# Performance work log

Hardware: AMD Instinct MI355X
Metric: run time of the kernel (lower is better)

The kernel has to match this reference:

```python
import jax, jax.numpy as jnp
import numpy as np

# ---- static synthetic forest: 64 complete binary trees, depth 9 (heap layout) ----
DEPTH = 9
N_TREES = 64
C = 8
M = 256
N_GEN = 8
NPT = 2 ** (DEPTH + 1) - 1          # 1023 nodes per tree
DIM = N_TREES * NPT                  # 65472 total nodes
_base = np.arange(N_TREES) * NPT

def _lvl_nodes(l):
    return (_base[:, None] + np.arange(2 ** l - 1, 2 ** (l + 1) - 1)[None, :]).reshape(-1)

LEVELS = []   # list of (parent_idx, child_idx) edge arrays, top level first
UPAR = []     # unique parents per level (== nodes of level l-1)
for _l in range(1, DEPTH + 1):
    _ch = np.arange(2 ** _l - 1, 2 ** (_l + 1) - 1)
    _pa = (_ch - 1) // 2
    LEVELS.append((jnp.asarray((_base[:, None] + _pa[None, :]).reshape(-1)),
                   jnp.asarray((_base[:, None] + _ch[None, :]).reshape(-1))))
    UPAR.append(jnp.asarray(_lvl_nodes(_l - 1)))
LEAVES = jnp.asarray(_lvl_nodes(DEPTH))
ROOTS = jnp.asarray(_base)
INTERNAL = jnp.asarray(np.concatenate([_lvl_nodes(l) for l in range(DEPTH)]))
TREES_IND = jnp.asarray(np.repeat(np.arange(N_TREES), NPT))
N_CH = 2.0  # every internal node has exactly 2 children -> segment mean = sum/2


def _forward(A, B, Pi, x):
    # softmax reparameterization (per generative head)
    sm_A = jax.nn.softmax(A, axis=0)          # (C,C,G), softmax over parent-state dim 0
    sm_B = jax.nn.softmax(B, axis=1)          # (C,M,G), softmax over symbols
    sm_Pi = jax.nn.softmax(Pi, axis=0)        # (C,G)

    # B[:, x] gathered per node, as (node, C, G)
    B_x = jnp.transpose(sm_B[:, x], (1, 0, 2))  # (DIM,C,G)

    # ---- reversed upward (leaves -> roots) ----
    beta = jnp.zeros((DIM, C, N_GEN), dtype=A.dtype)
    t_beta = jnp.zeros((DIM, C, N_GEN), dtype=A.dtype)
    b_leaf = sm_Pi[None, :, :] * B_x[LEAVES]                 # (L,C,G)
    beta = beta.at[LEAVES].set(b_leaf / b_leaf.sum(1, keepdims=True))
    for (pa, ch), upar in zip(reversed(LEVELS), reversed(UPAR)):
        beta_ch = beta[ch]                                   # (E,C,G)
        t_beta_ch = jnp.einsum('ijg,ejg->eig', sm_A, beta_ch)
        t_beta = t_beta + jax.ops.segment_sum(t_beta_ch, pa, num_segments=DIM) / N_CH
        beta_l = t_beta[upar] * B_x[upar]                    # (U,C,G)
        beta = beta.at[upar].set(beta_l / beta_l.sum(1, keepdims=True))

    # ---- reversed downward (roots -> leaves) ----
    eps = jnp.zeros((DIM, C, N_GEN), dtype=A.dtype)
    t_eps = jnp.zeros((DIM, C, C, N_GEN), dtype=A.dtype)
    eps = eps.at[ROOTS].set(beta[ROOTS])
    for pa, ch in LEVELS:
        # (E,Cpa,Cch,G)
        eps_joint = (eps[pa][:, :, None, :] * sm_A[None]
                     * beta[ch][:, None, :, :] / t_beta[pa][:, :, None, :])
        t_eps = t_eps + jax.ops.segment_sum(eps_joint, pa, num_segments=DIM) / N_CH
        eps = eps.at[ch].set(eps_joint.sum(1))

    # ---- log-likelihood ----
    lik = jnp.zeros((DIM, N_GEN), dtype=A.dtype)
    lik = lik.at[INTERNAL].add((t_eps[INTERNAL] * jnp.log(sm_A)[None]).sum((1, 2)))
    lik = lik + (eps * jnp.log(B_x)).sum(1)  # all_nodes == all nodes here
    lik = lik.at[LEAVES].add((eps[LEAVES] * jnp.log(sm_Pi)[None]).sum(1))
    ll = jax.ops.segment_sum(lik, TREES_IND, num_segments=N_TREES)  # (n_trees,G)
    return -ll


def setup_inputs() -> dict:
    key = jax.random.key(0)
    k1, k2, k3, k4 = jax.random.split(key, 4)
    A = jax.random.uniform(k1, (C, C, N_GEN), minval=-5.0, maxval=5.0)
    B = jax.random.uniform(k2, (C, M, N_GEN), minval=-5.0, maxval=5.0)
    Pi = jax.random.uniform(k3, (C, N_GEN), minval=-5.0, maxval=5.0)
    x = jax.random.randint(k4, (DIM,), 0, M)
    return {"A": A, "B": B, "Pi": Pi, "x": x}


def reference(A, B, Pi, x):
    return _forward(A, B, Pi, x)
```

## Files before the change

kernel.cpp:

```cpp
#include <hip/hip_runtime.h>

#define NT 256

namespace {
constexpr int C = 8, G = 8, M = 256, NPT = 1023;
constexpr int PD = 12;

__device__ __forceinline__ float rcpf(float x) { return __builtin_amdgcn_rcpf(x); }

#define LD8(dst, srcp) do {                                              \
    const float4 _a = *(const float4*)(srcp);                            \
    const float4 _b = *(const float4*)((srcp) + 4);                      \
    (dst)[0]=_a.x;(dst)[1]=_a.y;(dst)[2]=_a.z;(dst)[3]=_a.w;             \
    (dst)[4]=_b.x;(dst)[5]=_b.y;(dst)[6]=_b.z;(dst)[7]=_b.w; } while(0)

#define ST8(dstp, src) do {                                              \
    *(float4*)(dstp)       = make_float4((src)[0],(src)[1],(src)[2],(src)[3]); \
    *(float4*)((dstp) + 4) = make_float4((src)[4],(src)[5],(src)[6],(src)[7]); } while(0)

__global__ __launch_bounds__(NT, 2)
void htmm_fused(const float* __restrict__ Ag, const float* __restrict__ Bg,
                const float* __restrict__ Pig, const int* __restrict__ xg,
                float* __restrict__ out)
{
    __shared__ int xs[NPT + 1];
    __shared__ __align__(16) float smBt[M][PD];
    __shared__ __align__(16) float logBt[M][PD];
    __shared__ __align__(16) float bet[511][PD];
    __shared__ __align__(16) float tbe[255][PD];
    __shared__ __align__(16) float smA_s[C][C];
    __shared__ __align__(16) float alA_s[C][C];
    __shared__ float pi_s[2][C];
    __shared__ float red[4];

    const int tid  = threadIdx.x;
    const int wv   = tid >> 6, lane = tid & 63;
    const int tree = blockIdx.x >> 3, g = blockIdx.x & 7;

    for (int n = tid; n < NPT; n += NT) xs[n] = xg[tree * NPT + n];
    {
        const int i  = 2 * wv + (lane >> 5);
        const int c0 = lane & 31;
        float raw[8], ex[8], ssum = 0.f;
        #pragma unroll
        for (int t = 0; t < 8; ++t) {
            raw[t] = Bg[(i * M + c0 + 32 * t) * G + g];
            ex[t]  = __expf(raw[t]);
            ssum  += ex[t];
        }
        #pragma unroll
        for (int m = 1; m <= 16; m <<= 1) ssum += __shfl_xor(ssum, m);
        const float inv = rcpf(ssum), ls = __logf(ssum);
        #pragma unroll
        for (int t = 0; t < 8; ++t) {
            smBt [c0 + 32 * t][i] = ex[t] * inv;
            logBt[c0 + 32 * t][i] = raw[t] - ls;
        }
    }
    if (wv == 0) {
        const int si = lane >> 3, qj = lane & 7;
        const float raw = Ag[(si * C + qj) * G + g];
        float e = __expf(raw), S = e;
        #pragma unroll
        for (int m = 8; m <= 32; m <<= 1) S += __shfl_xor(S, m);
        const float v = e / S;
        smA_s[si][qj] = v;
        alA_s[si][qj] = v * (raw - __logf(S));
    } else if (wv == 1 && lane < C) {
        const float raw = Pig[lane * G + g];
        float e = __expf(raw), S = e;
        #pragma unroll
        for (int m = 1; m <= 4; m <<= 1) S += __shfl_xor(S, m);
        pi_s[0][lane] = e / S;
        pi_s[1][lane] = raw - __logf(S);
    }
    __syncthreads();

    float Ae[64], ALAe[64], piR[8], lPi[8];
    #pragma unroll
    for (int i = 0; i < 8; ++i) {
        float ar[8], lr[8];
        LD8(ar, &smA_s[i][0]);
        LD8(lr, &alA_s[i][0]);
        #pragma unroll
        for (int j = 0; j < 8; ++j) { Ae[8*i+j] = ar[j]; ALAe[8*i+j] = lr[j]; }
    }
    #pragma unroll
    for (int i = 0; i < 8; ++i) { piR[i] = pi_s[0][i]; lPi[i] = pi_s[1][i]; }

    const int nd8 = 255 + tid;
    const int xv8 = xs[nd8], xvL = xs[2*nd8 + 1], xvR = xs[2*nd8 + 2];
    float bl0[8], bl1[8], tb8[8], b8[8];
    {
        float sm[8], u[8], S, inv;
        LD8(sm, &smBt[xvL][0]);
        S = 0.f;
        #pragma unroll
        for (int i = 0; i < 8; ++i) { u[i] = piR[i] * sm[i]; S += u[i]; }
        inv = rcpf(S);
        #pragma unroll
        for (int i = 0; i < 8; ++i) bl0[i] = u[i] * inv;

        LD8(sm, &smBt[xvR][0]);
        S = 0.f;
        #pragma unroll
        for (int i = 0; i < 8; ++i) { u[i] = piR[i] * sm[i]; S += u[i]; }
        inv = rcpf(S);
        #pragma unroll
        for (int i = 0; i < 8; ++i) bl1[i] = u[i] * inv;

        float c[8];
        #pragma unroll
        for (int j = 0; j < 8; ++j) c[j] = bl0[j] + bl1[j];
        #pragma unroll
        for (int i = 0; i < 8; ++i) {
            float t = 0.f;
            #pragma unroll
            for (int j = 0; j < 8; ++j) t += Ae[8*i+j] * c[j];
            tb8[i] = 0.5f * t;
        }
        LD8(sm, &smBt[xv8][0]);
        S = 0.f;
        #pragma unroll
        for (int i = 0; i < 8; ++i) { u[i] = tb8[i] * sm[i]; S += u[i]; }
        inv = rcpf(S);
        #pragma unroll
        for (int i = 0; i < 8; ++i) b8[i] = u[i] * inv;
        ST8(&bet[nd8][0], b8);
    }
    __syncthreads();

    for (int lvl = 7; lvl >= 0; --lvl) {
        const int cnt = 1 << lvl, base = cnt - 1;
        if (tid < cnt) {
            const int p = base + tid, cl = 2*p + 1;
            float lb_[8], rb_[8], cb[8];
            LD8(lb_, &bet[cl][0]);
            LD8(rb_, &bet[cl + 1][0]);
            #pragma unroll
            for (int j = 0; j < 8; ++j) cb[j] = lb_[j] + rb_[j];
            float tb[8];
            #pragma unroll
            for (int i = 0; i < 8; ++i) {
                float t = 0.f;
                #pragma unroll
                for (int j = 0; j < 8; ++j) t += Ae[8*i+j] * cb[j];
                tb[i] = 0.5f * t;
            }
            ST8(&tbe[p][0], tb);
            float sm[8], u[8], S = 0.f;
            LD8(sm, &smBt[xs[p]][0]);
            #pragma unroll
            for (int i = 0; i < 8; ++i) { u[i] = tb[i] * sm[i]; S += u[i]; }
            const float inv = rcpf(S);
            float b[8];
            #pragma unroll
            for (int i = 0; i < 8; ++i) b[i] = u[i] * inv;
            ST8(&bet[p][0], b);
        }
        __syncthreads();
    }

    float acc = 0.f;
    if (tid == 0) {
        float b0[8], lb[8];
        LD8(b0, &bet[0][0]);
        LD8(lb, &logBt[xs[0]][0]);
        #pragma unroll
        for (int j = 0; j < 8; ++j) acc += b0[j] * lb[j];
    }

    for (int dc = 1; dc <= 7; ++dc) {
        const int cnt = 1 << dc, base = cnt - 1;
        if (tid < cnt) {
            const int ch = base + tid, p = (ch - 1) >> 1;
            float ep[8], tp[8], w[8];
            LD8(ep, &bet[p][0]);
            LD8(tp, &tbe[p][0]);
            #pragma unroll
            for (int i = 0; i < 8; ++i) w[i] = ep[i] * rcpf(tp[i]);
            float es[8] = {0,0,0,0,0,0,0,0}, ts[8] = {0,0,0,0,0,0,0,0};
            #pragma unroll
            for (int i = 0; i < 8; ++i) {
                #pragma unroll
                for (int j = 0; j < 8; ++j) {
                    es[j] += w[i] * Ae[8*i+j];
                    ts[j] += w[i] * ALAe[8*i+j];
                }
            }
            float bc[8], lb[8], ev[8];
            LD8(bc, &bet[ch][0]);
            LD8(lb, &logBt[xs[ch]][0]);
            float a1 = 0.f, a2 = 0.f;
            #pragma unroll
            for (int j = 0; j < 8; ++j) {
                ev[j] = bc[j] * es[j];
                a1 += bc[j] * ts[j];
                a2 += ev[j] * lb[j];
            }
            acc += 0.5f * a1 + a2;
            ST8(&bet[ch][0], ev);
        }
        __syncthreads();
    }

    {
        const int p7 = (nd8 - 1) >> 1;
        float ep[8], tp[8], w[8];
        LD8(ep, &bet[p7][0]);
        LD8(tp, &tbe[p7][0]);
        #pragma unroll
        for (int i = 0; i < 8; ++i) w[i] = ep[i] * rcpf(tp[i]);
        float es[8] = {0,0,0,0,0,0,0,0}, ts[8] = {0,0,0,0,0,0,0,0};
        #pragma unroll
        for (int i = 0; i < 8; ++i) {
            #pragma unroll
            for (int j = 0; j < 8; ++j) {
                es[j] += w[i] * Ae[8*i+j];
                ts[j] += w[i] * ALAe[8*i+j];
            }
        }
        float lb[8], ev8[8], w8[8];
        LD8(lb, &logBt[xv8][0]);
        float a1 = 0.f, a2 = 0.f;
        #pragma unroll
        for (int j = 0; j < 8; ++j) {
            ev8[j] = b8[j] * es[j];
            a1 += b8[j] * ts[j];
            a2 += ev8[j] * lb[j];
        }
        acc += 0.5f * a1 + a2;
        #pragma unroll
        for (int i = 0; i < 8; ++i) w8[i] = ev8[i] * rcpf(tb8[i]);

        float es2[8] = {0,0,0,0,0,0,0,0}, ts2[8] = {0,0,0,0,0,0,0,0};
        #pragma unroll
        for (int i = 0; i < 8; ++i) {
            #pragma unroll
            for (int j = 0; j < 8; ++j) {
                es2[j] += w8[i] * Ae[8*i+j];
                ts2[j] += w8[i] * ALAe[8*i+j];
            }
        }
        LD8(lb, &logBt[xvL][0]);
        a1 = 0.f; a2 = 0.f;
        #pragma unroll
        for (int j = 0; j < 8; ++j) {
            const float ev = bl0[j] * es2[j];
            a1 += bl0[j] * ts2[j];
            a2 += ev * (lb[j] + lPi[j]);
        }
        acc += 0.5f * a1 + a2;
        LD8(lb, &logBt[xvR][0]);
        a1 = 0.f; a2 = 0.f;
        #pragma unroll
        for (int j = 0; j < 8; ++j) {
            const float ev = bl1[j] * es2[j];
            a1 += bl1[j] * ts2[j];
            a2 += ev * (lb[j] + lPi[j]);
        }
        acc += 0.5f * a1 + a2;
    }

    #pragma unroll
    for (int m = 1; m <= 32; m <<= 1) acc += __shfl_xor(acc, m);
    if (lane == 0) red[wv] = acc;
    __syncthreads();
    if (tid == 0) out[blockIdx.x] = -(red[0] + red[1] + red[2] + red[3]);
}
}

extern "C" void kernel_launch(void* const* d_in, const int* in_sizes, int n_in,
                              void* d_out, int out_size, void* d_ws, size_t ws_size,
                              hipStream_t stream) {
    const float* A  = (const float*)d_in[0];
    const float* Bm = (const float*)d_in[1];
    const float* Pi = (const float*)d_in[2];
    const int*   x  = (const int*)d_in[3];
    float* o = (float*)d_out;
    hipLaunchKernelGGL(htmm_fused, dim3(64 * 8), dim3(NT), 0, stream,
                       A, Bm, Pi, x, o);
}
```

Measured before the change: 90.02 us.

## Read transition matrices from LDS instead of registers and process child pairs per parent

Stops holding the 64-entry A and log-A matrices in per-thread registers and reads rows from shared memory (broadcast) inside helper lambdas, which should cut register pressure. The downward pass now has one thread per parent handle both children, so the weighted expectation (es/ts) is computed once per parent instead of twice. The trade-off is more LDS traffic per matrix-vector product, and the downward pass uses half as many active threads per level.

```diff
diff --git a/kernel.cpp b/kernel.cpp
--- a/kernel.cpp
+++ b/kernel.cpp
@@ -76,22 +76,36 @@
     }
     __syncthreads();
 
-    float Ae[64], ALAe[64], piR[8], lPi[8];
-    #pragma unroll
-    for (int i = 0; i < 8; ++i) {
-        float ar[8], lr[8];
-        LD8(ar, &smA_s[i][0]);
-        LD8(lr, &alA_s[i][0]);
-        #pragma unroll
-        for (int j = 0; j < 8; ++j) { Ae[8*i+j] = ar[j]; ALAe[8*i+j] = lr[j]; }
-    }
-    #pragma unroll
-    for (int i = 0; i < 8; ++i) { piR[i] = pi_s[0][i]; lPi[i] = pi_s[1][i]; }
+    auto trans_up = [&](const float* c8, float* tb) {
+        #pragma unroll
+        for (int i = 0; i < 8; ++i) {
+            float r[8]; LD8(r, &smA_s[i][0]);
+            float t = 0.f;
+            #pragma unroll
+            for (int j = 0; j < 8; ++j) t += r[j] * c8[j];
+            tb[i] = 0.5f * t;
+        }
+    };
+    auto wexp = [&](const float* w, float* es, float* ts) {
+        #pragma unroll
+        for (int j = 0; j < 8; ++j) { es[j] = 0.f; ts[j] = 0.f; }
+        #pragma unroll
+        for (int i = 0; i < 8; ++i) {
+            float a[8], l[8];
+            LD8(a, &smA_s[i][0]);
+            LD8(l, &alA_s[i][0]);
+            #pragma unroll
+            for (int j = 0; j < 8; ++j) { es[j] += w[i] * a[j]; ts[j] += w[i] * l[j]; }
+        }
+    };
+
+    float acc = 0.f;
 
     const int nd8 = 255 + tid;
     const int xv8 = xs[nd8], xvL = xs[2*nd8 + 1], xvR = xs[2*nd8 + 2];
     float bl0[8], bl1[8], tb8[8], b8[8];
     {
+        float piR[8]; LD8(piR, &pi_s[0][0]);
         float sm[8], u[8], S, inv;
         LD8(sm, &smBt[xvL][0]);
         S = 0.f;
@@ -112,13 +126,7 @@
         float c[8];
         #pragma unroll
         for (int j = 0; j < 8; ++j) c[j] = bl0[j] + bl1[j];
-        #pragma unroll
-        for (int i = 0; i < 8; ++i) {
-            float t = 0.f;
-            #pragma unroll
-            for (int j = 0; j < 8; ++j) t += Ae[8*i+j] * c[j];
-            tb8[i] = 0.5f * t;
-        }
+        trans_up(c, tb8);
         LD8(sm, &smBt[xv8][0]);
         S = 0.f;
         #pragma unroll
@@ -134,19 +142,12 @@
         const int cnt = 1 << lvl, base = cnt - 1;
         if (tid < cnt) {
             const int p = base + tid, cl = 2*p + 1;
-            float lb_[8], rb_[8], cb[8];
+            float lb_[8], rb_[8], cb[8], tb[8];
             LD8(lb_, &bet[cl][0]);
             LD8(rb_, &bet[cl + 1][0]);
             #pragma unroll
             for (int j = 0; j < 8; ++j) cb[j] = lb_[j] + rb_[j];
-            float tb[8];
-            #pragma unroll
-            for (int i = 0; i < 8; ++i) {
-                float t = 0.f;
-                #pragma unroll
-                for (int j = 0; j < 8; ++j) t += Ae[8*i+j] * cb[j];
-                tb[i] = 0.5f * t;
-            }
+            trans_up(cb, tb);
             ST8(&tbe[p][0], tb);
             float sm[8], u[8], S = 0.f;
             LD8(sm, &smBt[xs[p]][0]);
@@ -161,7 +162,6 @@
         __syncthreads();
     }
 
-    float acc = 0.f;
     if (tid == 0) {
         float b0[8], lb[8];
         LD8(b0, &bet[0][0]);
@@ -171,55 +171,44 @@
     }
 
     for (int dc = 1; dc <= 7; ++dc) {
-        const int cnt = 1 << dc, base = cnt - 1;
-        if (tid < cnt) {
-            const int ch = base + tid, p = (ch - 1) >> 1;
-            float ep[8], tp[8], w[8];
+        const int cntp = 1 << (dc - 1), basep = cntp - 1;
+        if (tid < cntp) {
+            const int p = basep + tid;
+            float ep[8], tp[8], w[8], es[8], ts[8];
             LD8(ep, &bet[p][0]);
             LD8(tp, &tbe[p][0]);
             #pragma unroll
             for (int i = 0; i < 8; ++i) w[i] = ep[i] * rcpf(tp[i]);
-            float es[8] = {0,0,0,0,0,0,0,0}, ts[8] = {0,0,0,0,0,0,0,0};
-            #pragma unroll
-            for (int i = 0; i < 8; ++i) {
+            wexp(w, es, ts);
+            #pragma unroll
+            for (int cc = 0; cc < 2; ++cc) {
+                const int ch = 2*p + 1 + cc;
+                float bc[8], lb[8], ev[8];
+                LD8(bc, &bet[ch][0]);
+                LD8(lb, &logBt[xs[ch]][0]);
+                float a1 = 0.f, a2 = 0.f;
                 #pragma unroll
                 for (int j = 0; j < 8; ++j) {
-                    es[j] += w[i] * Ae[8*i+j];
-                    ts[j] += w[i] * ALAe[8*i+j];
+                    ev[j] = bc[j] * es[j];
+                    a1 += bc[j] * ts[j];
+                    a2 += ev[j] * lb[j];
                 }
+                acc += 0.5f * a1 + a2;
+                ST8(&bet[ch][0], ev);
             }
-            float bc[8], lb[8], ev[8];
-            LD8(bc, &bet[ch][0]);
-            LD8(lb, &logBt[xs[ch]][0]);
-            float a1 = 0.f, a2 = 0.f;
-            #pragma unroll
-            for (int j = 0; j < 8; ++j) {
-                ev[j] = bc[j] * es[j];
-                a1 += bc[j] * ts[j];
-                a2 += ev[j] * lb[j];
-            }
-            acc += 0.5f * a1 + a2;
-            ST8(&bet[ch][0], ev);
         }
         __syncthreads();
     }
 
     {
         const int p7 = (nd8 - 1) >> 1;
-        float ep[8], tp[8], w[8];
+        float ep[8], tp[8], w[8], es[8], ts[8];
         LD8(ep, &bet[p7][0]);
         LD8(tp, &tbe[p7][0]);
         #pragma unroll
         for (int i = 0; i < 8; ++i) w[i] = ep[i] * rcpf(tp[i]);
-        float es[8] = {0,0,0,0,0,0,0,0}, ts[8] = {0,0,0,0,0,0,0,0};
-        #pragma unroll
-        for (int i = 0; i < 8; ++i) {
-            #pragma unroll
-            for (int j = 0; j < 8; ++j) {
-                es[j] += w[i] * Ae[8*i+j];
-                ts[j] += w[i] * ALAe[8*i+j];
-            }
-        }
+        wexp(w, es, ts);
+
         float lb[8], ev8[8], w8[8];
         LD8(lb, &logBt[xv8][0]);
         float a1 = 0.f, a2 = 0.f;
@@ -233,21 +222,14 @@
         #pragma unroll
         for (int i = 0; i < 8; ++i) w8[i] = ev8[i] * rcpf(tb8[i]);
 
-        float es2[8] = {0,0,0,0,0,0,0,0}, ts2[8] = {0,0,0,0,0,0,0,0};
-        #pragma unroll
-        for (int i = 0; i < 8; ++i) {
-            #pragma unroll
-            for (int j = 0; j < 8; ++j) {
-                es2[j] += w8[i] * Ae[8*i+j];
-                ts2[j] += w8[i] * ALAe[8*i+j];
-            }
-        }
+        wexp(w8, es, ts);
+        float lPi[8]; LD8(lPi, &pi_s[1][0]);
         LD8(lb, &logBt[xvL][0]);
         a1 = 0.f; a2 = 0.f;
         #pragma unroll
         for (int j = 0; j < 8; ++j) {
-            const float ev = bl0[j] * es2[j];
-            a1 += bl0[j] * ts2[j];
+            const float ev = bl0[j] * es[j];
+            a1 += bl0[j] * ts[j];
             a2 += ev * (lb[j] + lPi[j]);
         }
         acc += 0.5f * a1 + a2;
@@ -255,8 +237,8 @@
         a1 = 0.f; a2 = 0.f;
         #pragma unroll
         for (int j = 0; j < 8; ++j) {
-            const float ev = bl1[j] * es2[j];
-            a1 += bl1[j] * ts2[j];
+            const float ev = bl1[j] * es[j];
+            a1 += bl1[j] * ts[j];
             a2 += ev * (lb[j] + lPi[j]);
         }
         acc += 0.5f * a1 + a2;
```

Result: faster. 77.99 us (-13.4%).
